# Kernel optimization log

Hardware: AMD Instinct MI355X
Metric: run time of the kernel (lower is better)

Reference implementation:

```python
import jax, jax.numpy as jnp
import numpy as np

B, S, D = 4, 4096, 2048
DECAY_BIAS_INIT = -4.0
W_SCALE = 0.02


def setup_inputs() -> dict:
    key = jax.random.key(0)
    ks = jax.random.split(key, 6)
    return {
        "x": jax.random.normal(ks[0], (B, S, D), dtype=jnp.float32),
        "W_in": jax.random.normal(ks[1], (D, D), dtype=jnp.float32) * W_SCALE,
        "b_in": jnp.zeros((D,), jnp.float32),
        "W_decay": jax.random.normal(ks[2], (D, D), dtype=jnp.float32) * W_SCALE,
        "b_decay": jnp.zeros((D,), jnp.float32),
        "W_gate": jax.random.normal(ks[3], (D, D), dtype=jnp.float32) * W_SCALE,
        "b_gate": jnp.zeros((D,), jnp.float32),
        "W_out": jax.random.normal(ks[4], (D, D), dtype=jnp.float32) * W_SCALE,
        "b_out": jnp.zeros((D,), jnp.float32),
        "decay_bias": jnp.full((D,), DECAY_BIAS_INIT, jnp.float32),
    }


def reference(x, W_in, b_in, W_decay, b_decay, W_gate, b_gate, W_out, b_out, decay_bias):
    # Projections (weights stored as [in, out]; torch Linear applies x @ W.T, here W is pre-transposed)
    inp = jax.nn.silu(jnp.einsum("bsd,de->bse", x, W_in) + b_in).astype(jnp.float32)
    decay = jax.nn.sigmoid(jnp.einsum("bsd,de->bse", x, W_decay) + b_decay + decay_bias)
    gate = jax.nn.sigmoid(jnp.einsum("bsd,de->bse", x, W_gate) + b_gate)

    # Gated linear recurrence: s_t = d_t * s_{t-1} + (1 - d_t) * i_t
    def step(state, di):
        d, i = di
        state = d * state + (1.0 - d) * i
        return state, state

    init = jnp.zeros((x.shape[0], x.shape[2]), jnp.float32)
    _, states = jax.lax.scan(
        step, init, (jnp.swapaxes(decay, 0, 1), jnp.swapaxes(inp, 0, 1))
    )  # states: [S, B, D]
    y = gate * jnp.swapaxes(states, 0, 1)  # [B, S, D]
    y = y.astype(x.dtype)
    return jnp.einsum("bsd,de->bse", y, W_out) + b_out
```

## Files before the change

### kernel.cpp

```cpp
#include <hip/hip_runtime.h>

typedef unsigned short u16;
typedef __attribute__((ext_vector_type(4))) float f4;
typedef __attribute__((ext_vector_type(8))) short s8v;
typedef __attribute__((ext_vector_type(8))) unsigned short u16x8;
typedef __attribute__((ext_vector_type(4))) unsigned short u16x4;

#define B_   4
#define S_   4096
#define D_   2048
#define M_   (B_ * S_)
#define K_   D_
#define N3_  (3 * D_)
#define CCH  128
#define LCH  32
#define NTK  32

__device__ __forceinline__ u16 f2bf(float f) {
  unsigned u = __float_as_uint(f);
  u += 0x7FFF + ((u >> 16) & 1);
  return (u16)(u >> 16);
}
__device__ __forceinline__ float bf2f(u16 h) {
  return __uint_as_float(((unsigned)h) << 16);
}
__device__ __forceinline__ float sigm(float z) {
  return 1.0f / (1.0f + __expf(-z));
}

__global__ void k_cvt(const float* __restrict__ src, u16* __restrict__ dst, int n4) {
  int i = blockIdx.x * 256 + threadIdx.x;
  if (i >= n4) return;
  f4 v = *(const f4*)(src + (size_t)i * 4);
  u16x4 o;
  o[0] = f2bf(v[0]); o[1] = f2bf(v[1]); o[2] = f2bf(v[2]); o[3] = f2bf(v[3]);
  *(u16x4*)(dst + (size_t)i * 4) = o;
}

__global__ void k_tcvt4(const float* __restrict__ W_in, const float* __restrict__ W_dec,
                        const float* __restrict__ W_gate, const float* __restrict__ W_out,
                        u16* __restrict__ w3t, u16* __restrict__ wot) {
  __shared__ float tile[32][33];
  const float* src = (blockIdx.z == 0) ? W_in : (blockIdx.z == 1) ? W_dec
                    : (blockIdx.z == 2) ? W_gate : W_out;
  u16* dst = (blockIdx.z < 3) ? (w3t + (size_t)blockIdx.z * 2048 * 2048) : wot;
  int tx = threadIdx.x & 31, ty = threadIdx.x >> 5;
  int c0 = blockIdx.x * 32, r0 = blockIdx.y * 32;
#pragma unroll
  for (int j = 0; j < 32; j += 8)
    tile[ty + j][tx] = src[(size_t)(r0 + ty + j) * 2048 + c0 + tx];
  __syncthreads();
#pragma unroll
  for (int j = 0; j < 32; j += 8)
    dst[(size_t)(c0 + ty + j) * 2048 + r0 + tx] = f2bf(tile[tx][ty + j]);
}

__global__ void __launch_bounds__(512, 2)
k_gemm256(const u16* __restrict__ A, const u16* __restrict__ BT, int N, int mode,
          u16* __restrict__ o_inp, u16* __restrict__ o_dec, u16* __restrict__ o_gate,
          const float* __restrict__ b_in, const float* __restrict__ b_dec,
          const float* __restrict__ b_gate, const float* __restrict__ dbias,
          float* __restrict__ o_f, const float* __restrict__ b_out) {
  extern __shared__ u16 smem[];
  u16* const Asb[2] = { smem,         smem + 16384 };
  u16* const Bsb[2] = { smem + 32768, smem + 49152 };

  const int bid = blockIdx.x;
  const int xcd = bid & 7, j = bid >> 3;
  const int nsb = j >> 6;
  const int rj = j & 63;
  const int mm = rj >> 3, nn = rj & 7;
  const int tile_m = ((xcd << 3) + mm) << 8;
  const int tile_n = ((nsb << 3) + nn) << 8;

  const int tid = threadIdx.x;
  const int wave = tid >> 6, lane = tid & 63;
  const int wm = (wave >> 2) << 7;
  const int wn = (wave & 3) << 6;
  const int l15 = lane & 15, lhi = lane >> 4;
  const int srow = tid >> 3, sslot = tid & 7;

  f4 acc[8][4];
#pragma unroll
  for (int m = 0; m < 8; ++m)
#pragma unroll
    for (int n = 0; n < 4; ++n)
#pragma unroll
      for (int r = 0; r < 4; ++r) acc[m][n][r] = 0.0f;

  s8v afr2[2][2][2];
  s8v bfr[2][4];

  const int swz = l15 & 7;
  const u16* ap[2][2];
  const u16* bp[2][2];
#pragma unroll
  for (int b = 0; b < 2; ++b)
#pragma unroll
    for (int kk = 0; kk < 2; ++kk) {
      const int so = ((((kk << 2) + lhi) ^ swz) << 3);
      ap[b][kk] = Asb[b] + ((wm + l15) << 6) + so;
      bp[b][kk] = Bsb[b] + ((wn + l15) << 6) + so;
    }
  const int gl = srow * K_ + ((sslot ^ (srow & 7)) << 3);

  auto STAGE = [&](const u16* __restrict__ G, int grow0, u16* L, int c, int k0) {
    const u16* src = G + (size_t)(grow0 + (c << 6)) * K_ + k0;
    __builtin_amdgcn_global_load_lds(
        (const __attribute__((address_space(1))) unsigned int*)(src + gl),
        (__attribute__((address_space(3))) unsigned int*)(L + (((c << 6) + (wave << 3)) << 6)),
        16, 0, 0);
  };

#pragma unroll
  for (int c = 0; c < 4; ++c) STAGE(A, tile_m, Asb[0], c, 0);
#pragma unroll
  for (int c = 0; c < 4; ++c) STAGE(BT, tile_n, Bsb[0], c, 0);
#pragma unroll
  for (int c = 0; c < 4; ++c) STAGE(BT, tile_n, Bsb[1], c, 64);
  STAGE(A, tile_m, Asb[1], 0, 64);
  STAGE(A, tile_m, Asb[1], 2, 64);
  asm volatile("s_waitcnt vmcnt(6)" ::: "memory");
  __builtin_amdgcn_s_barrier();

#pragma unroll
  for (int kk = 0; kk < 2; ++kk)
#pragma unroll
    for (int mi = 0; mi < 2; ++mi)
      afr2[0][mi][kk] = *(const s8v*)(ap[0][kk] + (mi << 10));
#pragma unroll
  for (int kk = 0; kk < 2; ++kk)
#pragma unroll
    for (int n = 0; n < 4; ++n)
      bfr[kk][n] = *(const s8v*)(bp[0][kk] + (n << 10));

#pragma unroll 1
  for (int it = 0; it < NTK / 2; ++it) {
    const int t0 = it << 1;
#pragma unroll
    for (int p = 0; p < 8; ++p) {
      const int toff[8] = {1, 2, 2, 2, 2, 3, 3, 3};
      const int sopA[8] = {1, 0, 0, 1, 1, 0, 0, 1};
      const int sc0[8]  = {1, 0, 2, 0, 1, 0, 2, 0};
      const int sc1f[8] = {3, 1, 3, 2, 3, 1, 3, 2};
      const int q = p & 3;

      {
        const int st = (t0 + toff[p]) & (NTK - 1);
        const int k0s = st << 6;
        u16* const Ad = Asb[st & 1];
        u16* const Bd = Bsb[st & 1];
        if (sopA[p]) { STAGE(A, tile_m, Ad, sc0[p], k0s); STAGE(A, tile_m, Ad, sc1f[p], k0s); }
        else         { STAGE(BT, tile_n, Bd, sc0[p], k0s); STAGE(BT, tile_n, Bd, sc1f[p], k0s); }
      }
      if (q == 3) {
        asm volatile("s_waitcnt vmcnt(6)" ::: "memory");
        __builtin_amdgcn_sched_barrier(0);
      }
      __builtin_amdgcn_s_barrier();

      {
        const int pn = p + 1;
        const int qn = pn & 3, bn = (pn >> 2) & 1, as = pn & 1;
#pragma unroll
        for (int kk = 0; kk < 2; ++kk)
#pragma unroll
          for (int mi = 0; mi < 2; ++mi)
            afr2[as][mi][kk] = *(const s8v*)(ap[bn][kk] + (((qn << 1) + mi) << 10));
      }

      __builtin_amdgcn_s_setprio(1);
#pragma unroll
      for (int kk = 0; kk < 2; ++kk)
#pragma unroll
        for (int mi = 0; mi < 2; ++mi)
#pragma unroll
          for (int n = 0; n < 4; ++n)
            acc[q * 2 + mi][n] =
                __builtin_amdgcn_mfma_f32_16x16x32_bf16(afr2[p & 1][mi][kk], bfr[kk][n],
                                                        acc[q * 2 + mi][n], 0, 0, 0);
      __builtin_amdgcn_s_setprio(0);

      if (q == 3) {
        const int bn = ((p + 1) >> 2) & 1;
#pragma unroll
        for (int kk = 0; kk < 2; ++kk)
#pragma unroll
          for (int n = 0; n < 4; ++n)
            bfr[kk][n] = *(const s8v*)(bp[bn][kk] + (n << 10));
      }
    }
  }

  asm volatile("s_waitcnt vmcnt(0)" ::: "memory");
  __builtin_amdgcn_s_barrier();

  if (mode == 0) {
    const int selb = tile_n >> 11;
    const int dbase = tile_n & 2047;
    float bias[4];
#pragma unroll
    for (int n = 0; n < 4; ++n) {
      int d = dbase + wn + (n << 4) + l15;
      bias[n] = (selb == 0) ? b_in[d] : (selb == 1) ? (b_dec[d] + dbias[d]) : b_gate[d];
    }
#pragma unroll
    for (int m = 0; m < 8; ++m)
#pragma unroll
      for (int n = 0; n < 4; ++n)
#pragma unroll
        for (int r = 0; r < 4; ++r) {
          int lrow = wm + (m << 4) + (lhi << 2) + r;
          int lcol = wn + (n << 4) + l15;
          float z = acc[m][n][r] + bias[n];
          float v = (selb == 0) ? z * sigm(z) : sigm(z);
          smem[(lrow << 8) + (((lcol >> 3) ^ (lrow & 7)) << 3) + (lcol & 7)] = f2bf(v);
        }
    __builtin_amdgcn_s_barrier();
    u16* const dst = (selb == 0) ? o_inp : (selb == 1) ? o_dec : o_gate;
    const int rr = tid >> 5, sl = tid & 31;
#pragma unroll
    for (int pass = 0; pass < 16; ++pass) {
      int row = (pass << 4) + rr;
      u16x8 v = *(const u16x8*)(smem + (row << 8) + ((sl ^ (row & 7)) << 3));
      *(u16x8*)(dst + (size_t)(tile_m + row) * D_ + dbase + (sl << 3)) = v;
    }
  } else {
    float* const Tf = (float*)smem;
    f4 bo = *(const f4*)(b_out + tile_n + (lane << 2));
#pragma unroll
    for (int sw = 0; sw < 2; ++sw) {
      if (sw) __builtin_amdgcn_s_barrier();
      if ((wm >> 7) == sw) {
#pragma unroll
        for (int m = 0; m < 8; ++m)
#pragma unroll
          for (int n = 0; n < 4; ++n)
#pragma unroll
            for (int r = 0; r < 4; ++r) {
              int lrow = (m << 4) + (lhi << 2) + r;
              int lcol = wn + (n << 4) + l15;
              Tf[(lrow << 8) + (((lcol >> 2) ^ (lrow & 7)) << 2) + (lcol & 3)] = acc[m][n][r];
            }
      }
      __builtin_amdgcn_s_barrier();
#pragma unroll
      for (int pass = 0; pass < 16; ++pass) {
        int lrow = (pass << 3) + wave;
        f4 v = *(const f4*)(Tf + (lrow << 8) + ((lane ^ (lrow & 7)) << 2));
        v[0] += bo[0]; v[1] += bo[1]; v[2] += bo[2]; v[3] += bo[3];
        *(f4*)(o_f + (size_t)(tile_m + (sw << 7) + lrow) * D_ + tile_n + (lane << 2)) = v;
      }
    }
  }
}

__global__ void k_scan1(const u16* __restrict__ dec, const u16* __restrict__ inp,
                        float* __restrict__ chA, float* __restrict__ chB) {
  int b = blockIdx.x / CCH, c = blockIdx.x % CCH;
  int d0 = threadIdx.x * 8;
  const u16* dp = dec + ((size_t)b * S_ + c * LCH) * D_ + d0;
  const u16* ip = inp + ((size_t)b * S_ + c * LCH) * D_ + d0;
  float Aa[8], st[8];
#pragma unroll
  for (int i = 0; i < 8; ++i) { Aa[i] = 1.0f; st[i] = 0.0f; }
#pragma unroll 4
  for (int j = 0; j < LCH; ++j) {
    u16x8 dv = *(const u16x8*)(dp + (size_t)j * D_);
    u16x8 iv = *(const u16x8*)(ip + (size_t)j * D_);
#pragma unroll
    for (int i = 0; i < 8; ++i) {
      float dd = bf2f(dv[i]), ii = bf2f(iv[i]);
      Aa[i] *= dd;
      st[i] = dd * st[i] + (1.0f - dd) * ii;
    }
  }
  size_t o = ((size_t)b * CCH + c) * D_ + d0;
#pragma unroll
  for (int i = 0; i < 8; ++i) { chA[o + i] = Aa[i]; chB[o + i] = st[i]; }
}

__global__ void k_scan2(const float* __restrict__ chA, const float* __restrict__ chB,
                        float* __restrict__ ini) {
  int b = blockIdx.x >> 3;
  int d = ((blockIdx.x & 7) << 8) + threadIdx.x;
  float st = 0.0f;
  for (int c = 0; c < CCH; ++c) {
    size_t o = ((size_t)b * CCH + c) * D_ + d;
    ini[o] = st;
    st = chA[o] * st + chB[o];
  }
}

__global__ void k_scan3(const u16* __restrict__ dec, const u16* __restrict__ inp,
                        const u16* __restrict__ gat, const float* __restrict__ ini,
                        u16* __restrict__ y) {
  int b = blockIdx.x / CCH, c = blockIdx.x % CCH;
  int d0 = threadIdx.x * 8;
  size_t ib = ((size_t)b * CCH + c) * D_ + d0;
  float st[8];
#pragma unroll
  for (int i = 0; i < 8; ++i) st[i] = ini[ib + i];
  size_t base = ((size_t)b * S_ + c * LCH) * D_ + d0;
#pragma unroll 4
  for (int j = 0; j < LCH; ++j) {
    size_t o = base + (size_t)j * D_;
    u16x8 dv = *(const u16x8*)(dec + o);
    u16x8 iv = *(const u16x8*)(inp + o);
    u16x8 gv = *(const u16x8*)(gat + o);
    u16x8 yv;
#pragma unroll
    for (int i = 0; i < 8; ++i) {
      float dd = bf2f(dv[i]), ii = bf2f(iv[i]);
      st[i] = dd * st[i] + (1.0f - dd) * ii;
      yv[i] = f2bf(bf2f(gv[i]) * st[i]);
    }
    *(u16x8*)(y + o) = yv;
  }
}

extern "C" void kernel_launch(void* const* d_in, const int* in_sizes, int n_in,
                              void* d_out, int out_size, void* d_ws, size_t ws_size,
                              hipStream_t stream) {
  (void)in_sizes; (void)n_in; (void)out_size; (void)ws_size;
  const float* x      = (const float*)d_in[0];
  const float* W_in   = (const float*)d_in[1];
  const float* b_in   = (const float*)d_in[2];
  const float* W_dec  = (const float*)d_in[3];
  const float* b_dec  = (const float*)d_in[4];
  const float* W_gate = (const float*)d_in[5];
  const float* b_gate = (const float*)d_in[6];
  const float* W_out  = (const float*)d_in[7];
  const float* b_out  = (const float*)d_in[8];
  const float* dbias  = (const float*)d_in[9];
  float* out = (float*)d_out;

  char* ws = (char*)d_ws;
  u16*   xb  = (u16*)(ws);
  u16*   w3t = (u16*)(ws + 67108864ull);
  u16*   wot = (u16*)(ws + 92274688ull);
  u16*   inp = (u16*)(ws + 100663296ull);
  u16*   dec = (u16*)(ws + 167772160ull);
  u16*   gat = (u16*)(ws + 234881024ull);
  float* chA = (float*)(ws + 301989888ull);
  float* chB = (float*)(ws + 306184192ull);
  float* ini = (float*)(ws + 310378496ull);
  u16*   y   = xb;

  hipFuncSetAttribute((const void*)k_gemm256,
                      hipFuncAttributeMaxDynamicSharedMemorySize, 131072);

  k_cvt<<<32768, 256, 0, stream>>>(x, xb, 8388608);
  k_tcvt4<<<dim3(64, 64, 4), 256, 0, stream>>>(W_in, W_dec, W_gate, W_out, w3t, wot);

  k_gemm256<<<(M_ / 256) * (N3_ / 256), 512, 131072, stream>>>(
      xb, w3t, N3_, 0, inp, dec, gat, b_in, b_dec, b_gate, dbias, nullptr, nullptr);

  k_scan1<<<B_ * CCH, 256, 0, stream>>>(dec, inp, chA, chB);
  k_scan2<<<32, 256, 0, stream>>>(chA, chB, ini);
  k_scan3<<<B_ * CCH, 256, 0, stream>>>(dec, inp, gat, ini, y);

  k_gemm256<<<(M_ / 256) * (D_ / 256), 512, 131072, stream>>>(
      y, wot, D_, 1, nullptr, nullptr, nullptr, nullptr, nullptr, nullptr, nullptr,
      out, b_out);
}
```

Baseline: 636.5 us.

## Split chunk-carry scan into hierarchical three-level scan, grid-stride convert kernel

The serial pass over 128 chunk carries, run by only 32 blocks, is replaced by a two-level scan: 256 blocks reduce groups of 16 chunks, a small kernel scans the 8 group carries, and 256 blocks propagate the carries back to each chunk. This exposes more parallelism in a latency-bound stage at the cost of two extra launches and a small extra workspace. The input conversion kernel also becomes grid-stride with 2048 blocks instead of 32768.

```diff
diff --git a/kernel.cpp b/kernel.cpp
--- a/kernel.cpp
+++ b/kernel.cpp
@@ -15,6 +15,8 @@
 #define CCH  128
 #define LCH  32
 #define NTK  32
+#define SCH  8
+#define SCL  16
 
 __device__ __forceinline__ u16 f2bf(float f) {
   unsigned u = __float_as_uint(f);
@@ -29,12 +31,12 @@
 }
 
 __global__ void k_cvt(const float* __restrict__ src, u16* __restrict__ dst, int n4) {
-  int i = blockIdx.x * 256 + threadIdx.x;
-  if (i >= n4) return;
-  f4 v = *(const f4*)(src + (size_t)i * 4);
-  u16x4 o;
-  o[0] = f2bf(v[0]); o[1] = f2bf(v[1]); o[2] = f2bf(v[2]); o[3] = f2bf(v[3]);
-  *(u16x4*)(dst + (size_t)i * 4) = o;
+  for (int i = blockIdx.x * 256 + threadIdx.x; i < n4; i += 2048 * 256) {
+    f4 v = *(const f4*)(src + (size_t)i * 4);
+    u16x4 o;
+    o[0] = f2bf(v[0]); o[1] = f2bf(v[1]); o[2] = f2bf(v[2]); o[3] = f2bf(v[3]);
+    *(u16x4*)(dst + (size_t)i * 4) = o;
+  }
 }
 
 __global__ void k_tcvt4(const float* __restrict__ W_in, const float* __restrict__ W_dec,
@@ -280,13 +282,45 @@
   for (int i = 0; i < 8; ++i) { chA[o + i] = Aa[i]; chB[o + i] = st[i]; }
 }
 
-__global__ void k_scan2(const float* __restrict__ chA, const float* __restrict__ chB,
-                        float* __restrict__ ini) {
-  int b = blockIdx.x >> 3;
-  int d = ((blockIdx.x & 7) << 8) + threadIdx.x;
+__global__ void k_scan2a(const float* __restrict__ chA, const float* __restrict__ chB,
+                         float* __restrict__ sA, float* __restrict__ sB) {
+  int gid = blockIdx.x * 256 + threadIdx.x;
+  int d = gid & (D_ - 1);
+  int s = (gid >> 11) & (SCH - 1);
+  int b = gid >> 14;
+  float Aa = 1.0f, Bb = 0.0f;
+  for (int c = 0; c < SCL; ++c) {
+    size_t o = ((size_t)b * CCH + s * SCL + c) * D_ + d;
+    float a = chA[o], bb = chB[o];
+    Aa *= a;
+    Bb = a * Bb + bb;
+  }
+  size_t so = ((size_t)b * SCH + s) * D_ + d;
+  sA[so] = Aa; sB[so] = Bb;
+}
+
+__global__ void k_scan2b(const float* __restrict__ sA, const float* __restrict__ sB,
+                         float* __restrict__ sI) {
+  int gid = blockIdx.x * 256 + threadIdx.x;
+  int d = gid & (D_ - 1);
+  int b = gid >> 11;
   float st = 0.0f;
-  for (int c = 0; c < CCH; ++c) {
-    size_t o = ((size_t)b * CCH + c) * D_ + d;
+  for (int s = 0; s < SCH; ++s) {
+    size_t o = ((size_t)b * SCH + s) * D_ + d;
+    sI[o] = st;
+    st = sA[o] * st + sB[o];
+  }
+}
+
+__global__ void k_scan2c(const float* __restrict__ chA, const float* __restrict__ chB,
+                         const float* __restrict__ sI, float* __restrict__ ini) {
+  int gid = blockIdx.x * 256 + threadIdx.x;
+  int d = gid & (D_ - 1);
+  int s = (gid >> 11) & (SCH - 1);
+  int b = gid >> 14;
+  float st = sI[((size_t)b * SCH + s) * D_ + d];
+  for (int c = 0; c < SCL; ++c) {
+    size_t o = ((size_t)b * CCH + s * SCL + c) * D_ + d;
     ini[o] = st;
     st = chA[o] * st + chB[o];
   }
@@ -345,19 +379,24 @@
   float* chA = (float*)(ws + 301989888ull);
   float* chB = (float*)(ws + 306184192ull);
   float* ini = (float*)(ws + 310378496ull);
+  float* sA  = (float*)(ws + 314572800ull);
+  float* sB  = (float*)(ws + 314834944ull);
+  float* sI  = (float*)(ws + 315097088ull);
   u16*   y   = xb;
 
   hipFuncSetAttribute((const void*)k_gemm256,
                       hipFuncAttributeMaxDynamicSharedMemorySize, 131072);
 
-  k_cvt<<<32768, 256, 0, stream>>>(x, xb, 8388608);
+  k_cvt<<<2048, 256, 0, stream>>>(x, xb, 8388608);
   k_tcvt4<<<dim3(64, 64, 4), 256, 0, stream>>>(W_in, W_dec, W_gate, W_out, w3t, wot);
 
   k_gemm256<<<(M_ / 256) * (N3_ / 256), 512, 131072, stream>>>(
       xb, w3t, N3_, 0, inp, dec, gat, b_in, b_dec, b_gate, dbias, nullptr, nullptr);
 
   k_scan1<<<B_ * CCH, 256, 0, stream>>>(dec, inp, chA, chB);
-  k_scan2<<<32, 256, 0, stream>>>(chA, chB, ini);
+  k_scan2a<<<256, 256, 0, stream>>>(chA, chB, sA, sB);
+  k_scan2b<<<32, 256, 0, stream>>>(sA, sB, sI);
+  k_scan2c<<<256, 256, 0, stream>>>(chA, chB, sI, ini);
   k_scan3<<<B_ * CCH, 256, 0, stream>>>(dec, inp, gat, ini, y);
 
   k_gemm256<<<(M_ / 256) * (D_ / 256), 512, 131072, stream>>>(
```

New measurement: 631.8 us (median of 2 runs). About the same (-0.7%).
